# Kernel optimization log

Hardware: AMD Instinct MI355X
Metric: run time of the kernel (lower is better)

Reference implementation:

```python
import jax, jax.numpy as jnp
import numpy as np


def _run_stacked_lstm(x, init_hc, params):
    """x: [B,T,E]; init_hc: tuple of (h,c) per layer; params: tuple of (W,U,b) per layer.
    Keras LSTMCell gate order: i, f, g(candidate), o; sigmoid recurrent act, tanh act."""
    def step(carry, xt):
        inp = xt
        new = []
        for (h, c), (W, U, b) in zip(carry, params):
            z = inp @ W + h @ U + b                      # [B, 4*units]
            i, f, g, o = jnp.split(z, 4, axis=-1)
            c2 = jax.nn.sigmoid(f) * c + jax.nn.sigmoid(i) * jnp.tanh(g)
            h2 = jax.nn.sigmoid(o) * jnp.tanh(c2)
            new.append((h2, c2))
            inp = h2                                     # feed to next layer
        return tuple(new), inp
    carry, ys = jax.lax.scan(step, init_hc, jnp.swapaxes(x, 0, 1))
    return jnp.swapaxes(ys, 0, 1), carry                 # [B,T,units], final states


def setup_inputs() -> dict:
    key = jax.random.key(0)
    ks = jax.random.split(key, 20)
    B, T, V, E, H, L = 16, 64, 32000, 512, 512, 2
    s = 0.02
    inp = {
        'ids_1': jax.random.randint(ks[0], (B, T), 0, V),
        'ids_2': jax.random.randint(ks[1], (B, T), 0, V),
        'init_state': jax.random.normal(ks[2], (L, B, H), jnp.float32),
        'emb': jax.random.normal(ks[3], (V, E), jnp.float32) * s,
        'W1_0': jax.random.normal(ks[4], (E, 4 * H), jnp.float32) * s,
        'U1_0': jax.random.normal(ks[5], (H, 4 * H), jnp.float32) * s,
        'b1_0': jnp.zeros((4 * H,), jnp.float32),
        'W1_1': jax.random.normal(ks[6], (H, 4 * H), jnp.float32) * s,
        'U1_1': jax.random.normal(ks[7], (H, 4 * H), jnp.float32) * s,
        'b1_1': jnp.zeros((4 * H,), jnp.float32),
        'W2_0': jax.random.normal(ks[8], (E, 8 * H), jnp.float32) * s,
        'U2_0': jax.random.normal(ks[9], (2 * H, 8 * H), jnp.float32) * s,
        'b2_0': jnp.zeros((8 * H,), jnp.float32),
        'W2_1': jax.random.normal(ks[10], (2 * H, 8 * H), jnp.float32) * s,
        'U2_1': jax.random.normal(ks[11], (2 * H, 8 * H), jnp.float32) * s,
        'b2_1': jnp.zeros((8 * H,), jnp.float32),
        'Wp1': jax.random.normal(ks[12], (H, V), jnp.float32) * s,
        'bp1': jnp.zeros((V,), jnp.float32),
        'Wp2': jax.random.normal(ks[13], (2 * H, V), jnp.float32) * s,
        'bp2': jnp.zeros((V,), jnp.float32),
    }
    return inp


def reference(ids_1, ids_2, init_state, emb,
              W1_0, U1_0, b1_0, W1_1, U1_1, b1_1,
              W2_0, U2_0, b2_0, W2_1, U2_1, b2_1,
              Wp1, bp1, Wp2, bp2):
    L = init_state.shape[0]
    e1 = emb[ids_1]                                       # [B,T,E]
    e2 = emb[ids_2]
    # RNN1: initial (h,c) both set to init_state per layer
    init1 = tuple((init_state[l], init_state[l]) for l in range(L))
    p1 = ((W1_0, U1_0, b1_0), (W1_1, U1_1, b1_1))
    out1, st1 = _run_stacked_lstm(e1, init1, p1)
    logits1 = out1 @ Wp1 + bp1                            # [B,T,V]
    # RNN2: initial h = concat(init, h1_final), c = concat(init, c1_final)
    init2 = tuple((jnp.concatenate([init_state[l], st1[l][0]], axis=1),
                   jnp.concatenate([init_state[l], st1[l][1]], axis=1))
                  for l in range(L))
    p2 = ((W2_0, U2_0, b2_0), (W2_1, U2_1, b2_1))
    out2, _ = _run_stacked_lstm(e2, init2, p2)
    logits2 = out2 @ Wp2 + bp2                            # [B,T,V]
    return (logits1, logits2)
```

## Files before the change

### kernel.cpp

```cpp
#include <hip/hip_runtime.h>
#include <hip/hip_bf16.h>

#define B_ 16
#define T_ 64
#define E_ 512
#define H_ 512
#define V_ 32000

typedef __attribute__((ext_vector_type(4))) float f32x4;
typedef __attribute__((ext_vector_type(8))) short s16x8;

__device__ __forceinline__ float sigm(float x){ return 1.0f/(1.0f + __expf(-x)); }

__device__ __forceinline__ unsigned short f2bf(float x){
  unsigned int u = __float_as_uint(x);
  return (unsigned short)((u + 0x7FFFu + ((u>>16)&1u)) >> 16);
}

__device__ __forceinline__ unsigned load_coh(const unsigned* p){
  unsigned v;
  asm volatile("global_load_dword %0, %1, off sc0 sc1\n\ts_waitcnt vmcnt(0)"
               : "=v"(v) : "v"(p) : "memory");
  return v;
}
__device__ __forceinline__ void store_coh16(unsigned short* p, unsigned v){
  asm volatile("global_store_short %0, %1, off sc0 sc1" :: "v"(p), "v"(v) : "memory");
}
__device__ __forceinline__ void store_cohf(float* p, float v){
  asm volatile("global_store_dword %0, %1, off sc0 sc1" :: "v"(p), "v"(v) : "memory");
}
__device__ __forceinline__ void store_cohu(unsigned* p, unsigned v){
  asm volatile("global_store_dword %0, %1, off sc0 sc1" :: "v"(p), "v"(v) : "memory");
}

__device__ __forceinline__ void gbar3(unsigned* barb, unsigned bi1, int nblk,
                                      bool det, int myblk){
  asm volatile("s_waitcnt vmcnt(0)" ::: "memory");
  __syncthreads();
  const int tid = threadIdx.x;
  if(tid == 0) store_cohu(barb + (size_t)myblk*16, bi1);
  if(det){
    if(tid < nblk){
      const unsigned* fp = barb + (size_t)tid*16;
      while(load_coh(fp) < bi1) __builtin_amdgcn_s_sleep(1);
    }
    __syncthreads();
    if(tid < 8) store_cohu(barb + 4096 + (size_t)tid*16, bi1);
  } else {
    if(tid == 0){
      const unsigned* gp = barb + 4096 + (size_t)(myblk & 7)*16;
      while(load_coh(gp) < bi1) __builtin_amdgcn_s_sleep(1);
    }
  }
  __syncthreads();
}

__global__ void k_barinit(unsigned* bar){
  int i = blockIdx.x*256 + threadIdx.x;
  if(i < 16384) bar[i] = 0u;
}

__global__ void k_gather(const int* __restrict__ ids, const float* __restrict__ emb,
                         unsigned short* __restrict__ out){
  const int row = blockIdx.x;
  const int id  = ids[row];
  float4 v = *(const float4*)(emb + (size_t)id*E_ + threadIdx.x*4);
  ushort4 o;
  o.x = f2bf(v.x); o.y = f2bf(v.y); o.z = f2bf(v.z); o.w = f2bf(v.w);
  *(ushort4*)(out + (size_t)row*E_ + threadIdx.x*4) = o;
}

__device__ __forceinline__ void tcvt_dev(const float* __restrict__ in,
    unsigned short* __restrict__ out, int N, int Hp, int Kfull, int koff, int swz,
    int bx, int by, float (*tile)[33]){
  const int n0 = bx*32, k0 = by*32;
  const int x = threadIdx.x & 31, y = threadIdx.x >> 5;
  __syncthreads();
  #pragma unroll
  for(int i=0;i<4;i++){
    int k = y + i*8;
    tile[k][x] = in[(size_t)(k0+k)*N + n0 + x];
  }
  __syncthreads();
  #pragma unroll
  for(int i=0;i<4;i++){
    int nl = y + i*8;
    int n  = n0 + nl;
    int p  = Hp ? ((n % Hp)*4 + n / Hp) : n;
    int kk = koff + k0 + x;
    size_t idx;
    if(swz){
      int k2 = kk*2;
      int slot = ((k2>>4)&7) ^ (p&7);
      idx = (size_t)p*Kfull + (((k2 & ~127) | (slot<<4) | (k2 & 15)) >> 1);
    } else {
      idx = (size_t)p*Kfull + kk;
    }
    out[idx] = f2bf(tile[x][nl]);
  }
}

__global__ __launch_bounds__(256)
void k_tcvt(const float* __restrict__ in, unsigned short* __restrict__ out,
            int N, int Hp, int Kfull, int koff, int swz){
  __shared__ float tile[32][33];
  tcvt_dev(in, out, N, Hp, Kfull, koff, swz, blockIdx.x, blockIdx.y, tile);
}

__global__ void k_bpack(const float* __restrict__ b, float* __restrict__ out, int H, int N){
  int p = blockIdx.x*256 + threadIdx.x;
  if(p < N) out[p] = b[(p&3)*H + (p>>2)];
}

__global__ void k_init1(const float* __restrict__ init_state,
                        unsigned short* h0i, float* c0i, unsigned short* h1i, float* c1i){
  int i = blockIdx.x*256 + threadIdx.x;
  if(i >= B_*H_) return;
  float v0 = init_state[i];
  float v1 = init_state[B_*H_ + i];
  h0i[i] = f2bf(v0); c0i[i] = v0;
  h1i[i] = f2bf(v1); c1i[i] = v1;
}

__global__ void k_init2(const float* __restrict__ init_state,
                        const unsigned short* __restrict__ h0seq1,
                        const unsigned short* __restrict__ h1seq1,
                        const float* __restrict__ c0f1, const float* __restrict__ c1f1,
                        unsigned short* h20i, unsigned short* h21i,
                        float* c20i, float* c21i){
  const int l = blockIdx.y;
  int i = blockIdx.x*256 + threadIdx.x;
  if(i >= B_*2*H_) return;
  const int r = i >> 10, j = i & 1023;
  unsigned short* ho = l ? h21i : h20i;
  float* co = l ? c21i : c20i;
  if(j < H_){
    float v = init_state[(size_t)l*B_*H_ + r*H_ + j];
    ho[i] = f2bf(v); co[i] = v;
  } else {
    const unsigned short* hs = l ? h1seq1 : h0seq1;
    const float* cf = l ? c1f1 : c0f1;
    ho[i] = hs[(size_t)((T_-1)*B_ + r)*H_ + (j - H_)];
    co[i] = cf[r*H_ + (j - H_)];
  }
}

__device__ __forceinline__ void mm_tile(const unsigned short* __restrict__ A,
    const unsigned short* __restrict__ Bt, const float* __restrict__ bias,
    float* __restrict__ C, int N, int K, int bm, int bn,
    unsigned short* As, unsigned short* Bs, int remap){
  const int tid = threadIdx.x;
  const int lane = tid & 63, w = tid >> 6;
  const int wm = (w>>1)*64, wn = (w&1)*64;
  const int l15 = lane & 15, kg = lane >> 4;
  f32x4 acc[4][4] = {};
  for(int k0=0; k0<K; k0+=64){
    __syncthreads();
    #pragma unroll
    for(int ch=0; ch<4; ch++){
      int off = ch*4096 + tid*16;
      int row = off >> 7;
      int s   = ((off >> 4) & 7) ^ (row & 7);
      __builtin_amdgcn_global_load_lds(
        (const __attribute__((address_space(1))) unsigned int*)(A + (size_t)(bm+row)*K + k0 + s*8),
        (__attribute__((address_space(3))) unsigned int*)((char*)As + off), 16, 0, 0);
    }
    #pragma unroll
    for(int ch=0; ch<4; ch++){
      int off = ch*4096 + tid*16;
      int row = off >> 7;
      int s   = ((off >> 4) & 7) ^ (row & 7);
      __builtin_amdgcn_global_load_lds(
        (const __attribute__((address_space(1))) unsigned int*)(Bt + (size_t)(bn+row)*K + k0 + s*8),
        (__attribute__((address_space(3))) unsigned int*)((char*)Bs + off), 16, 0, 0);
    }
    __syncthreads();
    #pragma unroll
    for(int q=0;q<2;q++){
      s16x8 af[4], bf[4];
      #pragma unroll
      for(int mt=0;mt<4;mt++){
        int row = wm + mt*16 + l15;
        int s = (q*4 + kg) ^ (row & 7);
        af[mt] = *(const s16x8*)(As + row*64 + s*8);
      }
      #pragma unroll
      for(int nt=0;nt<4;nt++){
        int row = wn + nt*16 + l15;
        int s = (q*4 + kg) ^ (row & 7);
        bf[nt] = *(const s16x8*)(Bs + row*64 + s*8);
      }
      #pragma unroll
      for(int mt=0;mt<4;mt++)
        #pragma unroll
        for(int nt=0;nt<4;nt++)
          acc[mt][nt] = __builtin_amdgcn_mfma_f32_16x16x32_bf16(af[mt], bf[nt], acc[mt][nt], 0, 0, 0);
    }
  }
  #pragma unroll
  for(int mt=0;mt<4;mt++){
    #pragma unroll
    for(int nt=0;nt<4;nt++){
      int col = bn + wn + nt*16 + l15;
      float bv = bias ? bias[col] : 0.f;
      #pragma unroll
      for(int e=0;e<4;e++){
        int row = bm + wm + mt*16 + kg*4 + e;
        int orow = remap ? ((row & 15)*T_ + (row >> 4)) : row;
        C[(size_t)orow*N + col] = acc[mt][nt][e] + bv;
      }
    }
  }
}

template<int BF32>
__global__ __launch_bounds__(256)
void k_mm(const unsigned short* __restrict__ A, const void* __restrict__ Bsrc,
          const float* __restrict__ bias, float* __restrict__ C,
          int M, int N, int K, int remap, int bm0){
  __shared__ __align__(16) unsigned short As[128*64];
  __shared__ __align__(16) unsigned short Bs[128*64];
  if(!BF32){
    mm_tile(A, (const unsigned short*)Bsrc, bias, C, N, K,
            bm0 + blockIdx.y*128, blockIdx.x*128, As, Bs, remap);
    return;
  }
  const int tid = threadIdx.x;
  const int lane = tid & 63, w = tid >> 6;
  const int wm = (w>>1)*64, wn = (w&1)*64;
  const int bm = bm0 + blockIdx.y*128, bn = blockIdx.x*128;
  const int l15 = lane & 15, kg = lane >> 4;
  f32x4 acc[4][4] = {};
  for(int k0=0; k0<K; k0+=64){
    __syncthreads();
    #pragma unroll
    for(int ch=0; ch<4; ch++){
      int off = ch*4096 + tid*16;
      int row = off >> 7;
      int s   = ((off >> 4) & 7) ^ (row & 7);
      __builtin_amdgcn_global_load_lds(
        (const __attribute__((address_space(1))) unsigned int*)(A + (size_t)(bm+row)*K + k0 + s*8),
        (__attribute__((address_space(3))) unsigned int*)((char*)As + off), 16, 0, 0);
    }
    {
      const float* Bf = (const float*)Bsrc;
      #pragma unroll
      for(int i=0;i<8;i++){
        int kl = (tid>>5) + i*8;
        int nl = (tid&31)*4;
        float4 v = *(const float4*)(Bf + (size_t)(k0+kl)*N + bn + nl);
        int slot = kl >> 3, kb = kl & 7;
        float vv[4] = {v.x, v.y, v.z, v.w};
        #pragma unroll
        for(int jj=0;jj<4;jj++){
          int n = nl + jj;
          Bs[n*64 + ((slot ^ (n&7))*8) + kb] = f2bf(vv[jj]);
        }
      }
    }
    __syncthreads();
    #pragma unroll
    for(int q=0;q<2;q++){
      s16x8 af[4], bf[4];
      #pragma unroll
      for(int mt=0;mt<4;mt++){
        int row = wm + mt*16 + l15;
        int s = (q*4 + kg) ^ (row & 7);
        af[mt] = *(const s16x8*)(As + row*64 + s*8);
      }
      #pragma unroll
      for(int nt=0;nt<4;nt++){
        int row = wn + nt*16 + l15;
        int s = (q*4 + kg) ^ (row & 7);
        bf[nt] = *(const s16x8*)(Bs + row*64 + s*8);
      }
      #pragma unroll
      for(int mt=0;mt<4;mt++)
        #pragma unroll
        for(int nt=0;nt<4;nt++)
          acc[mt][nt] = __builtin_amdgcn_mfma_f32_16x16x32_bf16(af[mt], bf[nt], acc[mt][nt], 0, 0, 0);
    }
  }
  #pragma unroll
  for(int mt=0;mt<4;mt++){
    #pragma unroll
    for(int nt=0;nt<4;nt++){
      int col = bn + wn + nt*16 + l15;
      float bv = bias ? bias[col] : 0.f;
      #pragma unroll
      for(int e=0;e<4;e++){
        int row = bm + wm + mt*16 + kg*4 + e;
        int orow = remap ? ((row & 15)*T_ + (row >> 4)) : row;
        C[(size_t)orow*N + col] = acc[mt][nt][e] + bv;
      }
    }
  }
}

template<int C, int K, int LAYER, int HU, int TB>
__device__ __forceinline__ void rnn_body(
    unsigned short* __restrict__ Uld, float* __restrict__ zp,
    const unsigned short* __restrict__ Uslice,
    const float* __restrict__ xw0, const float* __restrict__ bpk,
    const unsigned short* __restrict__ h0init, const unsigned short* __restrict__ h1init,
    const float* __restrict__ cinit,
    unsigned short* __restrict__ h0seq, unsigned short* __restrict__ h1seq,
    float* __restrict__ cfin, unsigned* bar, int cb, int nblk, bool det, int myblk)
{
  constexpr int KW = K/4, KS = KW/32, FR = C/16, UB = C/4;
  constexpr int K2 = K*2;
  constexpr int ITEMS = 16*UB;
  const int tid = threadIdx.x;
  const int lane = tid & 63, w = tid >> 6;
  const int l15 = lane & 15, kg = lane >> 4;

  constexpr int CP = (C*K2)/4096;
  #pragma unroll
  for(int i=0;i<CP;i++){
    __builtin_amdgcn_global_load_lds(
      (const __attribute__((address_space(1))) unsigned int*)((const char*)Uslice + i*4096 + tid*16),
      (__attribute__((address_space(3))) unsigned int*)((char*)Uld + i*4096 + tid*16), 16, 0, 0);
  }
  const int base_p = cb*C;
  const int base_u = cb*UB;
  float4 bvr = make_float4(0.f,0.f,0.f,0.f);
  int er = 0, eu = 0;
  if(tid < ITEMS){ er = tid / UB; eu = tid - er*UB; bvr = *(const float4*)(bpk + base_p + eu*4); }
  float creg = 0.f;
  unsigned short* hseqW = LAYER ? h1seq : h0seq;

  int cbyte[FR], cx[FR];
  #pragma unroll
  for(int f=0;f<FR;f++){ int c = f*16 + l15; cbyte[f] = c*K2; cx[f] = (c&7)<<4; }

  __syncthreads();

  for(int it = 0; it <= T_; ++it){
    const bool active = LAYER ? (it >= 1) : (it < T_);
    const int t = LAYER ? it-1 : it;
    if(active){
      const unsigned short* asrc;
      if constexpr(LAYER == 0){
        asrc = (t == 0) ? (h0init + l15*HU)
             : (h0seq + ((size_t)(TB ? ((t-1)*B_ + l15) : (l15*T_ + (t-1))))*HU);
      } else {
        if(w < 2){
          asrc = h0seq + ((size_t)(TB ? (t*B_ + l15) : (l15*T_ + t)))*HU;
        } else {
          asrc = ((t == 0) ? (h1init + l15*HU)
               : (h1seq + ((size_t)(TB ? ((t-1)*B_ + l15) : (l15*T_ + (t-1))))*HU)) - HU;
        }
      }
      f32x4 acc[FR];
      #pragma unroll
      for(int f=0;f<FR;f++) acc[f] = (f32x4){0.f,0.f,0.f,0.f};
      #pragma unroll
      for(int s=0;s<KS;s++){
        const int kel = w*KW + s*32 + kg*8;
        s16x8 a = *(const s16x8*)(asrc + kel);
        const int kb  = kel*2;
        const int kch = kb & ~127;
        const int ksl = (kb >> 4) & 7;
        #pragma unroll
        for(int f=0;f<FR;f++){
          const int ad = cbyte[f] + kch + ((ksl<<4) ^ cx[f]);
          s16x8 b = *(const s16x8*)((const char*)Uld + ad);
          acc[f] = __builtin_amdgcn_mfma_f32_16x16x32_bf16(a, b, acc[f], 0, 0, 0);
        }
      }
      #pragma unroll
      for(int f=0;f<FR;f++)
        #pragma unroll
        for(int e=0;e<4;e++)
          zp[(w*16 + kg*4 + e)*68 + f*16 + l15] = acc[f][e];
    }
    __syncthreads();
    if(active && tid < ITEMS){
      float4 z0 = *(const float4*)(zp + (     er)*68 + eu*4);
      float4 z1 = *(const float4*)(zp + (16 + er)*68 + eu*4);
      float4 z2 = *(const float4*)(zp + (32 + er)*68 + eu*4);
      float4 z3 = *(const float4*)(zp + (48 + er)*68 + eu*4);
      float si = z0.x+z1.x+z2.x+z3.x + bvr.x;
      float sf = z0.y+z1.y+z2.y+z3.y + bvr.y;
      float sg = z0.z+z1.z+z2.z+z3.z + bvr.z;
      float so = z0.w+z1.w+z2.w+z3.w + bvr.w;
      if constexpr(LAYER == 0){
        float4 xv = *(const float4*)(xw0 + ((size_t)(er*T_ + t))*(4*HU) + base_p + eu*4);
        si += xv.x; sf += xv.y; sg += xv.z; so += xv.w;
      }
      float cin = (t == 0) ? cinit[er*HU + base_u + eu] : creg;
      float c2 = sigm(sf)*cin + sigm(si)*tanhf(sg);
      float h2 = sigm(so)*tanhf(c2);
      creg = c2;
      size_t hrow = TB ? ((size_t)(t*B_ + er)) : ((size_t)(er*T_ + t));
      store_coh16(&hseqW[hrow*HU + base_u + eu], (unsigned)f2bf(h2));
      if(t == T_-1) store_cohf(&cfin[er*HU + base_u + eu], c2);
    }
    if(it < T_) gbar3(bar, (unsigned)(it+1), nblk, det, myblk);
  }
  asm volatile("s_waitcnt vmcnt(0)" ::: "memory");
  __syncthreads();
  if(tid == 0) store_cohu(bar + (size_t)myblk*16, (unsigned)(T_+1));
}

__global__ __launch_bounds__(256, 1)
void k_rnn1m(const unsigned short* __restrict__ Ut0, const unsigned short* __restrict__ WU1,
    const float* __restrict__ xw0, const float* __restrict__ bpk0, const float* __restrict__ bpk1,
    const unsigned short* __restrict__ h0init, const unsigned short* __restrict__ h1init,
    const float* __restrict__ c0init, const float* __restrict__ c1init,
    unsigned short* __restrict__ h0seq, unsigned short* __restrict__ h1seq,
    float* __restrict__ c0fin, float* __restrict__ c1fin, unsigned* bar,
    const int* __restrict__ ids2, const float* __restrict__ emb, unsigned short* __restrict__ ebuf2,
    const float* __restrict__ b2_0, const float* __restrict__ b2_1,
    float* __restrict__ bpk20, float* __restrict__ bpk21,
    const float* __restrict__ U2_0, unsigned short* __restrict__ ut0_2,
    const float* __restrict__ W2_0, unsigned short* __restrict__ wtmp2,
    const float* __restrict__ W2_1, const float* __restrict__ U2_1, unsigned short* __restrict__ wu1_2,
    const float* __restrict__ Wp1, unsigned short* __restrict__ wpT1,
    const float* __restrict__ bp1, float* __restrict__ out1, int wide)
{
  constexpr int HU = 512, C0 = 64, C1 = 64;
  constexpr int NB0 = 4*HU/C0;
  constexpr int NRNN = NB0 + 4*HU/C1;
  constexpr int NS = 256 - NRNN;
  __shared__ __align__(16) unsigned short Uld[65536];
  __shared__ __align__(16) float zred[64*68];
  const int blk = blockIdx.x;
  const int tid = threadIdx.x;
  if(blk < NB0){
    rnn_body<C0, HU, 0, HU, 1>(Uld, zred, Ut0 + (size_t)blk*C0*HU, xw0, bpk0,
        h0init, h1init, c0init, h0seq, h1seq, c0fin, bar, blk, NRNN, blk==0, blk);
  } else if(blk < NRNN){
    rnn_body<C1, 2*HU, 1, HU, 1>(Uld, zred, WU1 + (size_t)(blk-NB0)*C1*2*HU, nullptr, bpk1,
        h0init, h1init, c1init, h0seq, h1seq, c1fin, bar, blk-NB0, NRNN, false, blk);
  } else {
    const int q = blk - NRNN;
    float (*tile)[33] = (float(*)[33])Uld;
    unsigned short* As = Uld;
    unsigned short* Bs = Uld + 8192;
    volatile int* rdy = (volatile int*)((char*)Uld + 128000);
    const int J0 = 512, J1 = J0+32, J2 = J1+4096, J3 = J2+2048, J4 = J3+4096, J5 = J4+4096;
    const int totJ = wide ? (J5 + 16000) : J5;
    for(int j = q; j < totJ; j += NS){
      if(j < J0){
        int row = j*2 + (tid>>7);
        int id = ids2[row];
        float4 v = *(const float4*)(emb + (size_t)id*E_ + (tid&127)*4);
        ushort4 o; o.x=f2bf(v.x); o.y=f2bf(v.y); o.z=f2bf(v.z); o.w=f2bf(v.w);
        *(ushort4*)(ebuf2 + (size_t)row*E_ + (tid&127)*4) = o;
      } else if(j < J1){
        int jj = j - J0;
        const float* b = (jj < 16) ? b2_0 : b2_1;
        float* o = (jj < 16) ? bpk20 : bpk21;
        int p = (jj & 15)*256 + tid;
        o[p] = b[(p&3)*1024 + (p>>2)];
      } else if(j < J2){
        int r = j - J1; tcvt_dev(U2_0, ut0_2, 4096, 1024, 1024, 0, 1, r%128, r/128, tile);
      } else if(j < J3){
        int r = j - J2; tcvt_dev(W2_0, wtmp2, 4096, 1024, 512, 0, 0, r%128, r/128, tile);
      } else if(j < J4){
        int r = j - J3; tcvt_dev(W2_1, wu1_2, 4096, 1024, 2048, 0, 1, r%128, r/128, tile);
      } else if(j < J5){
        int r = j - J4; tcvt_dev(U2_1, wu1_2, 4096, 1024, 2048, 1024, 1, r%128, r/128, tile);
      } else {
        int r = j - J5; tcvt_dev(Wp1, wpT1, 32000, 0, 512, 0, 0, r%1000, r/1000, tile);
      }
    }
    if(!wide) return;
    __syncthreads();
    __threadfence();
    if(tid == 0)
      __hip_atomic_fetch_add(bar + 5120, 1u, __ATOMIC_RELAXED, __HIP_MEMORY_SCOPE_AGENT);
    if(tid == 0){
      while(load_coh(bar + 5120) < (unsigned)NS) __builtin_amdgcn_s_sleep(8);
    }
    __syncthreads();
    for(int g = 0; g < 8; ++g){
      const unsigned req = 8u*(unsigned)g + 9u;
      for(;;){
        if(tid == 0) *rdy = 1;
        __syncthreads();
        if(tid < 32){
          if(load_coh(bar + (size_t)(NB0 + tid)*16) < req) *rdy = 0;
        }
        __syncthreads();
        if(*rdy) break;
        __builtin_amdgcn_s_sleep(16);
      }
      for(int n = q; n < 250; n += NS)
        mm_tile(h1seq, wpT1, bp1, out1, V_, 512, g*128, n*128, As, Bs, 1);
    }
  }
}

__global__ __launch_bounds__(256, 1)
void k_rnn2m(const unsigned short* __restrict__ Ut0, const unsigned short* __restrict__ WU1,
    const float* __restrict__ xw0, const float* __restrict__ bpk0, const float* __restrict__ bpk1,
    const unsigned short* __restrict__ h0init, const unsigned short* __restrict__ h1init,
    const float* __restrict__ c0init, const float* __restrict__ c1init,
    unsigned short* __restrict__ h0seq, unsigned short* __restrict__ h1seq,
    float* __restrict__ c0fin, float* __restrict__ c1fin, unsigned* bar,
    const float* __restrict__ Wp2, unsigned short* __restrict__ wpT2,
    const float* __restrict__ bp2, float* __restrict__ out2, int wide)
{
  constexpr int HU = 1024, C0 = 64, C1 = 32;
  constexpr int NB0 = 4*HU/C0;
  constexpr int NRNN = NB0 + 4*HU/C1;
  constexpr int NS = 64;
  __shared__ __align__(16) unsigned short Uld[65536];
  __shared__ __align__(16) float zred[64*68];
  const int blk = blockIdx.x;
  const int tid = threadIdx.x;
  if(blk < NB0){
    rnn_body<C0, HU, 0, HU, 1>(Uld, zred, Ut0 + (size_t)blk*C0*HU, xw0, bpk0,
        h0init, h1init, c0init, h0seq, h1seq, c0fin, bar, blk, NRNN, blk==0, blk);
  } else if(blk < NRNN){
    rnn_body<C1, 2*HU, 1, HU, 1>(Uld, zred, WU1 + (size_t)(blk-NB0)*C1*2*HU, nullptr, bpk1,
        h0init, h1init, c1init, h0seq, h1seq, c1fin, bar, blk-NB0, NRNN, false, blk);
  } else if(wide){
    const int q = blk - NRNN;
    float (*tile)[33] = (float(*)[33])Uld;
    unsigned short* As = Uld;
    unsigned short* Bs = Uld + 8192;
    volatile int* rdy = (volatile int*)((char*)Uld + 128000);
    for(int j = q; j < 32000; j += NS)
      tcvt_dev(Wp2, wpT2, 32000, 0, 1024, 0, 0, j%1000, j/1000, tile);
    __syncthreads();
    __threadfence();
    if(tid == 0)
      __hip_atomic_fetch_add(bar + 5120, 1u, __ATOMIC_RELAXED, __HIP_MEMORY_SCOPE_AGENT);
    if(tid == 0){
      while(load_coh(bar + 5120) < (unsigned)NS) __builtin_amdgcn_s_sleep(8);
    }
    __syncthreads();
    for(int g = 0; g < 2; ++g){
      const unsigned req = 8u*(unsigned)g + 9u;
      for(;;){
        if(tid == 0) *rdy = 1;
        __syncthreads();
        if(tid < 128){
          if(load_coh(bar + (size_t)(NB0 + tid)*16) < req) *rdy = 0;
        }
        __syncthreads();
        if(*rdy) break;
        __builtin_amdgcn_s_sleep(16);
      }
      for(int n = q; n < 250; n += NS)
        mm_tile(h1seq, wpT2, bp2, out2, V_, 1024, g*128, n*128, As, Bs, 1);
    }
  }
}

extern "C" void kernel_launch(void* const* d_in, const int* in_sizes, int n_in,
                              void* d_out, int out_size, void* d_ws, size_t ws_size,
                              hipStream_t stream){
  const int*   ids1 = (const int*)d_in[0];
  const int*   ids2 = (const int*)d_in[1];
  const float* init = (const float*)d_in[2];
  const float* emb  = (const float*)d_in[3];
  const float* W1_0 = (const float*)d_in[4];
  const float* U1_0 = (const float*)d_in[5];
  const float* b1_0 = (const float*)d_in[6];
  const float* W1_1 = (const float*)d_in[7];
  const float* U1_1 = (const float*)d_in[8];
  const float* b1_1 = (const float*)d_in[9];
  const float* W2_0 = (const float*)d_in[10];
  const float* U2_0 = (const float*)d_in[11];
  const float* b2_0 = (const float*)d_in[12];
  const float* W2_1 = (const float*)d_in[13];
  const float* U2_1 = (const float*)d_in[14];
  const float* b2_1 = (const float*)d_in[15];
  const float* Wp1  = (const float*)d_in[16];
  const float* bp1  = (const float*)d_in[17];
  const float* Wp2  = (const float*)d_in[18];
  const float* bp2  = (const float*)d_in[19];
  float* out1 = (float*)d_out;
  float* out2 = out1 + (size_t)B_*T_*V_;

  char* base = (char*)d_ws;
  float*          xw    = (float*)(base);
  unsigned short* ut0_1 = (unsigned short*)(base + (16u<<20));
  unsigned short* wu1_1 = (unsigned short*)(base + (18u<<20));
  unsigned short* ut0_2 = (unsigned short*)(base + (22u<<20));
  unsigned short* wu1_2 = (unsigned short*)(base + (30u<<20));
  unsigned short* wtmp  = (unsigned short*)(base + (46u<<20));
  unsigned short* ebuf  = (unsigned short*)(base + (50u<<20));
  unsigned short* h0s1  = (unsigned short*)(base + (51u<<20));
  unsigned short* h1s1  = (unsigned short*)(base + (52u<<20));
  unsigned short* h0s2  = (unsigned short*)(base + (53u<<20));
  unsigned short* h1s2  = (unsigned short*)(base + (55u<<20));
  char* M = base + (57u<<20);
  unsigned short* h0i1 = (unsigned short*)(M);
  unsigned short* h1i1 = (unsigned short*)(M + 16384);
  float* c0i1 = (float*)(M + 32768);
  float* c1i1 = (float*)(M + 65536);
  unsigned short* h2i0 = (unsigned short*)(M + 98304);
  unsigned short* h2i1 = (unsigned short*)(M + 131072);
  float* c2i0 = (float*)(M + 163840);
  float* c2i1 = (float*)(M + 229376);
  float* c0f1 = (float*)(M + 294912);
  float* c1f1 = (float*)(M + 327680);
  float* c0f2 = (float*)(M + 360448);
  float* c1f2 = (float*)(M + 425984);
  float* bpk10 = (float*)(M + 491520);
  float* bpk11 = (float*)(M + 499712);
  float* bpk20 = (float*)(M + 507904);
  float* bpk21 = (float*)(M + 524288);
  unsigned* bar1 = (unsigned*)(M + 540672);
  unsigned* bar2 = (unsigned*)(M + 540672 + 32768);
  unsigned short* wpT1 = (unsigned short*)(base + (58u<<20));
  unsigned short* wpT2 = (unsigned short*)(base + (90u<<20));
  const size_t NEED_ALL = ((size_t)90u<<20) + (size_t)V_*1024*2;
  const bool wide = ws_size >= NEED_ALL;

  k_barinit<<<dim3(64), dim3(256), 0, stream>>>(bar1);

  k_init1<<<dim3(32), dim3(256), 0, stream>>>(init, h0i1, c0i1, h1i1, c1i1);
  k_gather<<<dim3(B_*T_), dim3(128), 0, stream>>>(ids1, emb, ebuf);
  k_tcvt<<<dim3(64, 16), dim3(256), 0, stream>>>(U1_0, ut0_1, 2048, 512, 512, 0, 1);
  k_tcvt<<<dim3(64, 16), dim3(256), 0, stream>>>(W1_0, wtmp,  2048, 512, 512, 0, 0);
  k_tcvt<<<dim3(64, 16), dim3(256), 0, stream>>>(W1_1, wu1_1, 2048, 512, 1024, 0, 1);
  k_tcvt<<<dim3(64, 16), dim3(256), 0, stream>>>(U1_1, wu1_1, 2048, 512, 1024, 512, 1);
  k_bpack<<<dim3(8),  dim3(256), 0, stream>>>(b1_0, bpk10, 512, 2048);
  k_bpack<<<dim3(8),  dim3(256), 0, stream>>>(b1_1, bpk11, 512, 2048);
  k_mm<0><<<dim3(16, 8), dim3(256), 0, stream>>>(ebuf, wtmp, nullptr, xw, 1024, 2048, 512, 0, 0);

  k_rnn1m<<<dim3(256), dim3(256), 0, stream>>>(ut0_1, wu1_1, xw, bpk10, bpk11,
      h0i1, h1i1, c0i1, c1i1, h0s1, h1s1, c0f1, c1f1, bar1,
      ids2, emb, ebuf, b2_0, b2_1, bpk20, bpk21,
      U2_0, ut0_2, W2_0, wtmp, W2_1, U2_1, wu1_2, Wp1, wpT1, bp1, out1, (int)wide);

  if(!wide){
    k_mm<1><<<dim3(250, 8), dim3(256), 0, stream>>>(h1s1, Wp1, bp1, out1, 1024, V_, 512, 1, 0);
  }

  k_mm<0><<<dim3(32, 8), dim3(256), 0, stream>>>(ebuf, wtmp, nullptr, xw, 1024, 4096, 512, 0, 0);
  k_init2<<<dim3(64, 2), dim3(256), 0, stream>>>(init, h0s1, h1s1, c0f1, c1f1,
                                                 h2i0, h2i1, c2i0, c2i1);

  k_rnn2m<<<dim3(256), dim3(256), 0, stream>>>(ut0_2, wu1_2, xw, bpk20, bpk21,
      h2i0, h2i1, c2i0, c2i1, h0s2, h1s2, c0f2, c1f2, bar2,
      Wp2, wpT2, bp2, out2, (int)wide);

  if(wide){
    k_mm<0><<<dim3(250, 6), dim3(256), 0, stream>>>(h1s2, wpT2, bp2, out2, 1024, V_, 1024, 1, 256);
  } else {
    k_mm<1><<<dim3(250, 8), dim3(256), 0, stream>>>(h1s2, Wp2, bp2, out2, 1024, V_, 1024, 1, 0);
  }
}
```

Measured before the change: 1.034 ms.

## Move Wp2 transpose and RNN2 input GEMM into RNN1 side blocks, widen tcvt

The side blocks of the RNN1 persistent kernel now also transpose and convert Wp2 to bf16, using a new wide 256-column transpose routine instead of 32x32 tiles. When workspace allows, they also compute the RNN2 input projection (xw2) into a separate buffer. This removes that standalone GEMM launch and the Wp2 conversion from the RNN2 kernel. RNN2's spare blocks can then cover six of eight output row groups in overlap with the recurrence, leaving a smaller tail projection kernel. The risk is extra load on RNN1 side blocks and a dependence on a larger workspace.

```diff
diff --git a/kernel.cpp b/kernel.cpp
--- a/kernel.cpp
+++ b/kernel.cpp
@@ -105,6 +105,28 @@
             int N, int Hp, int Kfull, int koff, int swz){
   __shared__ float tile[32][33];
   tcvt_dev(in, out, N, Hp, Kfull, koff, swz, blockIdx.x, blockIdx.y, tile);
+}
+
+__device__ __forceinline__ void tcvtw_dev(const float* __restrict__ in,
+    unsigned short* __restrict__ out, int N, int K, int bx, int by,
+    float (*tile)[257]){
+  const int tid = threadIdx.x;
+  const int n0 = bx*256, k0 = by*32;
+  const int row = tid >> 3, nc = (tid & 7)*32;
+  __syncthreads();
+  #pragma unroll
+  for(int j=0;j<8;j++){
+    float4 v = *(const float4*)(in + (size_t)(k0+row)*N + n0 + nc + j*4);
+    *(float4*)&tile[row][nc + j*4] = v;
+  }
+  __syncthreads();
+  __align__(16) unsigned short vals[32];
+  #pragma unroll
+  for(int k=0;k<32;k++) vals[k] = f2bf(tile[k][tid]);
+  unsigned short* op = out + (size_t)(n0+tid)*K + k0;
+  #pragma unroll
+  for(int j=0;j<4;j++)
+    *(uint4*)(op + j*8) = *(const uint4*)&vals[j*8];
 }
 
 __global__ void k_bpack(const float* __restrict__ b, float* __restrict__ out, int H, int N){
@@ -417,7 +439,9 @@
     const float* __restrict__ W2_0, unsigned short* __restrict__ wtmp2,
     const float* __restrict__ W2_1, const float* __restrict__ U2_1, unsigned short* __restrict__ wu1_2,
     const float* __restrict__ Wp1, unsigned short* __restrict__ wpT1,
-    const float* __restrict__ bp1, float* __restrict__ out1, int wide)
+    const float* __restrict__ Wp2, unsigned short* __restrict__ wpT2,
+    const float* __restrict__ bp1, float* __restrict__ out1,
+    float* __restrict__ xw2buf, int wide)
 {
   constexpr int HU = 512, C0 = 64, C1 = 64;
   constexpr int NB0 = 4*HU/C0;
@@ -435,12 +459,15 @@
         h0init, h1init, c1init, h0seq, h1seq, c1fin, bar, blk-NB0, NRNN, false, blk);
   } else {
     const int q = blk - NRNN;
-    float (*tile)[33] = (float(*)[33])Uld;
+    float (*tile)[33]   = (float(*)[33])Uld;
+    float (*tile2)[257] = (float(*)[257])Uld;
     unsigned short* As = Uld;
     unsigned short* Bs = Uld + 8192;
     volatile int* rdy = (volatile int*)((char*)Uld + 128000);
     const int J0 = 512, J1 = J0+32, J2 = J1+4096, J3 = J2+2048, J4 = J3+4096, J5 = J4+4096;
-    const int totJ = wide ? (J5 + 16000) : J5;
+    const int J6 = J5 + 2000;
+    const int J7 = J6 + 4000;
+    const int totJ = wide ? J7 : J5;
     for(int j = q; j < totJ; j += NS){
       if(j < J0){
         int row = j*2 + (tid>>7);
@@ -462,8 +489,10 @@
         int r = j - J3; tcvt_dev(W2_1, wu1_2, 4096, 1024, 2048, 0, 1, r%128, r/128, tile);
       } else if(j < J5){
         int r = j - J4; tcvt_dev(U2_1, wu1_2, 4096, 1024, 2048, 1024, 1, r%128, r/128, tile);
+      } else if(j < J6){
+        int r = j - J5; tcvtw_dev(Wp1, wpT1, 32000, 512, r%125, r/125, tile2);
       } else {
-        int r = j - J5; tcvt_dev(Wp1, wpT1, 32000, 0, 512, 0, 0, r%1000, r/1000, tile);
+        int r = j - J6; tcvtw_dev(Wp2, wpT2, 32000, 1024, r%125, r/125, tile2);
       }
     }
     if(!wide) return;
@@ -475,6 +504,10 @@
       while(load_coh(bar + 5120) < (unsigned)NS) __builtin_amdgcn_s_sleep(8);
     }
     __syncthreads();
+    if(xw2buf){
+      for(int t2 = q; t2 < 256; t2 += NS)
+        mm_tile(ebuf2, wtmp2, nullptr, xw2buf, 4096, 512, (t2>>5)*128, (t2&31)*128, As, Bs, 0);
+    }
     for(int g = 0; g < 8; ++g){
       const unsigned req = 8u*(unsigned)g + 9u;
       for(;;){
@@ -500,7 +533,7 @@
     const float* __restrict__ c0init, const float* __restrict__ c1init,
     unsigned short* __restrict__ h0seq, unsigned short* __restrict__ h1seq,
     float* __restrict__ c0fin, float* __restrict__ c1fin, unsigned* bar,
-    const float* __restrict__ Wp2, unsigned short* __restrict__ wpT2,
+    const unsigned short* __restrict__ wpT2,
     const float* __restrict__ bp2, float* __restrict__ out2, int wide)
 {
   constexpr int HU = 1024, C0 = 64, C1 = 32;
@@ -519,21 +552,10 @@
         h0init, h1init, c1init, h0seq, h1seq, c1fin, bar, blk-NB0, NRNN, false, blk);
   } else if(wide){
     const int q = blk - NRNN;
-    float (*tile)[33] = (float(*)[33])Uld;
     unsigned short* As = Uld;
     unsigned short* Bs = Uld + 8192;
     volatile int* rdy = (volatile int*)((char*)Uld + 128000);
-    for(int j = q; j < 32000; j += NS)
-      tcvt_dev(Wp2, wpT2, 32000, 0, 1024, 0, 0, j%1000, j/1000, tile);
-    __syncthreads();
-    __threadfence();
-    if(tid == 0)
-      __hip_atomic_fetch_add(bar + 5120, 1u, __ATOMIC_RELAXED, __HIP_MEMORY_SCOPE_AGENT);
-    if(tid == 0){
-      while(load_coh(bar + 5120) < (unsigned)NS) __builtin_amdgcn_s_sleep(8);
-    }
-    __syncthreads();
-    for(int g = 0; g < 2; ++g){
+    for(int g = 0; g < 6; ++g){
       const unsigned req = 8u*(unsigned)g + 9u;
       for(;;){
         if(tid == 0) *rdy = 1;
@@ -610,8 +632,12 @@
   unsigned* bar2 = (unsigned*)(M + 540672 + 32768);
   unsigned short* wpT1 = (unsigned short*)(base + (58u<<20));
   unsigned short* wpT2 = (unsigned short*)(base + (90u<<20));
-  const size_t NEED_ALL = ((size_t)90u<<20) + (size_t)V_*1024*2;
-  const bool wide = ws_size >= NEED_ALL;
+  float*          xw2  = (float*)(base + (153u<<20));
+  const size_t NEED_W  = ((size_t)90u<<20) + (size_t)V_*1024*2;
+  const size_t NEED_W2 = ((size_t)169u<<20);
+  const bool wide  = ws_size >= NEED_W;
+  const bool wide2 = ws_size >= NEED_W2;
+  float* xw2p = wide2 ? xw2 : xw;
 
   k_barinit<<<dim3(64), dim3(256), 0, stream>>>(bar1);
 
@@ -628,22 +654,25 @@
   k_rnn1m<<<dim3(256), dim3(256), 0, stream>>>(ut0_1, wu1_1, xw, bpk10, bpk11,
       h0i1, h1i1, c0i1, c1i1, h0s1, h1s1, c0f1, c1f1, bar1,
       ids2, emb, ebuf, b2_0, b2_1, bpk20, bpk21,
-      U2_0, ut0_2, W2_0, wtmp, W2_1, U2_1, wu1_2, Wp1, wpT1, bp1, out1, (int)wide);
+      U2_0, ut0_2, W2_0, wtmp, W2_1, U2_1, wu1_2,
+      Wp1, wpT1, Wp2, wpT2, bp1, out1,
+      (wide && wide2) ? xw2 : nullptr, (int)wide);
 
   if(!wide){
     k_mm<1><<<dim3(250, 8), dim3(256), 0, stream>>>(h1s1, Wp1, bp1, out1, 1024, V_, 512, 1, 0);
   }
-
-  k_mm<0><<<dim3(32, 8), dim3(256), 0, stream>>>(ebuf, wtmp, nullptr, xw, 1024, 4096, 512, 0, 0);
+  if(!wide || !wide2){
+    k_mm<0><<<dim3(32, 8), dim3(256), 0, stream>>>(ebuf, wtmp, nullptr, xw, 1024, 4096, 512, 0, 0);
+  }
   k_init2<<<dim3(64, 2), dim3(256), 0, stream>>>(init, h0s1, h1s1, c0f1, c1f1,
                                                  h2i0, h2i1, c2i0, c2i1);
 
-  k_rnn2m<<<dim3(256), dim3(256), 0, stream>>>(ut0_2, wu1_2, xw, bpk20, bpk21,
+  k_rnn2m<<<dim3(256), dim3(256), 0, stream>>>(ut0_2, wu1_2, xw2p, bpk20, bpk21,
       h2i0, h2i1, c2i0, c2i1, h0s2, h1s2, c0f2, c1f2, bar2,
-      Wp2, wpT2, bp2, out2, (int)wide);
+      wpT2, bp2, out2, (int)wide);
 
   if(wide){
-    k_mm<0><<<dim3(250, 6), dim3(256), 0, stream>>>(h1s2, wpT2, bp2, out2, 1024, V_, 1024, 1, 256);
+    k_mm<0><<<dim3(250, 2), dim3(256), 0, stream>>>(h1s2, wpT2, bp2, out2, 1024, V_, 1024, 1, 768);
   } else {
     k_mm<1><<<dim3(250, 8), dim3(256), 0, stream>>>(h1s2, Wp2, bp2, out2, 1024, V_, 1024, 1, 0);
   }
```

After: 1.029 ms. About the same (-0.5%).
